# Optimization experiments

Hardware: AMD Instinct MI355X
Metric: run time of the kernel (lower is better)

Reference implementation:

```python
import jax, jax.numpy as jnp
import numpy as np

RADIUS = 6
KERNEL = 2 * RADIUS + 1  # 13
TEMPERATURE = 0.07
EPS = 1e-12  # F.normalize eps


def setup_inputs() -> dict:
    key = jax.random.key(0)
    k1, k2 = jax.random.split(key)
    B, C, H, W = 4, 256, 128, 128
    f_a = jax.random.normal(k1, (B, C, H, W), dtype=jnp.float32)
    f_b = jax.random.normal(k2, (B, C, H, W), dtype=jnp.float32)
    return {"f_a": f_a, "f_b": f_b}


def _l2_normalize(x):
    # matches F.normalize(x, dim=1): x / max(||x||_2, eps)
    n = jnp.sqrt(jnp.sum(x * x, axis=1, keepdims=True))
    return x / jnp.maximum(n, EPS)


def reference(f_a, f_b):
    a = _l2_normalize(f_a)
    b = _l2_normalize(f_b)
    b_pad = jnp.pad(b, ((0, 0), (0, 0), (RADIUS, RADIUS), (RADIUS, RADIUS)))

    # offsets in the same (row-major ky, kx) order as F.unfold
    ky, kx = jnp.meshgrid(jnp.arange(KERNEL), jnp.arange(KERNEL), indexing="ij")
    offsets = jnp.stack([ky.ravel(), kx.ravel()], axis=-1)  # [K^2, 2]

    shape = f_a.shape  # (B, C, H, W)

    def step(carry, off):
        shifted = jax.lax.dynamic_slice(b_pad, (0, 0, off[0], off[1]), shape)
        c = jnp.einsum("bchw,bchw->bhw", a, shifted)
        return carry, c

    _, corr = jax.lax.scan(step, None, offsets)  # [K^2, B, H, W]
    corr = jnp.transpose(corr, (1, 0, 2, 3)) / TEMPERATURE  # [B, K^2, H, W]
    return corr
```

## Files before the change

### kernel.cpp

```cpp
#include <hip/hip_runtime.h>
#include <stdint.h>


typedef _Float16 half8 __attribute__((ext_vector_type(8)));
typedef _Float16 half2v __attribute__((ext_vector_type(2)));
typedef float floatx4 __attribute__((ext_vector_type(4)));

#define B_ 4
#define C_ 256
#define H_ 128
#define W_ 128
#define K2_ 169
#define INV_T 14.285714285714286f
#define KGS (H_ * W_ * 32)

static __device__ __forceinline__ void gload16(const void* g, void* l) {
  __builtin_amdgcn_global_load_lds((const __attribute__((address_space(1))) void*)g,
                                   (__attribute__((address_space(3))) void*)l, 16, 0, 0);
}

__global__ __launch_bounds__(256, 4) void nt_kernel(const float* __restrict__ fa,
                                                    const float* __restrict__ fb,
                                                    _Float16* __restrict__ an,
                                                    _Float16* __restrict__ bn) {
  __shared__ _Float16 tile[256 * 66];
  __shared__ float ps[16 * 64];
  __shared__ float invn[64];
  const int bid = blockIdx.x;
  const int wh = bid & 1, h = (bid >> 1) & 127, bb = (bid >> 8) & 3, tens = bid >> 10;
  const float* __restrict__ src = tens ? fb : fa;
  _Float16* __restrict__ dst = tens ? bn : an;
  const int t = threadIdx.x;
  const int f = t & 15, cp = t >> 4;

  const float* gs = src + (((size_t)bb * C_ + cp) * H_ + h) * W_ + wh * 64 + f * 4;

  floatx4 v[16];
  #pragma unroll
  for (int it = 0; it < 16; ++it)
    v[it] = *(const floatx4*)(gs + (size_t)it * 16 * H_ * W_);

  floatx4 ss0 = {0.f, 0.f, 0.f, 0.f}, ss1 = {0.f, 0.f, 0.f, 0.f};
  #pragma unroll
  for (int it = 0; it < 16; ++it) {
    if (it & 1) ss1 += v[it] * v[it]; else ss0 += v[it] * v[it];
    const int c = it * 16 + cp;
    const int s8 = ((c >> 5) & 7) * 8;
    _Float16* wp = tile + c * 66 + ((f * 4) ^ s8);
    half2v p0 = {(_Float16)v[it].x, (_Float16)v[it].y};
    half2v p1 = {(_Float16)v[it].z, (_Float16)v[it].w};
    *(half2v*)wp = p0;
    *(half2v*)(wp + 2) = p1;
  }
  const floatx4 ss = ss0 + ss1;
  *(floatx4*)(ps + cp * 64 + f * 4) = ss;
  __syncthreads();
  if (t < 64) {
    float s2 = 0.f;
    #pragma unroll
    for (int p = 0; p < 16; ++p) s2 += ps[p * 64 + t];
    invn[t] = 1.0f / fmaxf(sqrtf(s2), 1e-12f);
  }
  __syncthreads();

  const int seg = t >> 5, pr = t & 31;
  const float sc = tens ? 1.0f : INV_T;
  const float inv0 = invn[2 * pr] * sc, inv1 = invn[2 * pr + 1] * sc;
  const int ppr = pr ^ (4 * seg);
  _Float16 o0[32] __attribute__((aligned(16)));
  _Float16 o1[32] __attribute__((aligned(16)));
  #pragma unroll
  for (int j = 0; j < 32; ++j) {
    const int c = seg * 32 + j;
    const half2v d = *(const half2v*)(tile + c * 66 + ppr * 2);
    o0[j] = (_Float16)((float)d.x * inv0);
    o1[j] = (_Float16)((float)d.y * inv1);
  }
  _Float16* dp = dst + ((((size_t)bb * 8 + seg) * H_ + h) * W_ + wh * 64 + 2 * pr) * 32;
  #pragma unroll
  for (int q4 = 0; q4 < 4; ++q4) {
    *(uint4*)(dp + q4 * 8) = *(const uint4*)(o0 + q4 * 8);
    *(uint4*)(dp + 32 + q4 * 8) = *(const uint4*)(o1 + q4 * 8);
  }
}

union SmemU { _Float16 stage[2][16384]; float ostage[K2_ * 2 * 17]; };

__global__ __launch_bounds__(512, 4) void corr_kernel(const _Float16* __restrict__ an,
                                                      const _Float16* __restrict__ bn,
                                                      float* __restrict__ out) {
  __shared__ SmemU u;
  const int bid = blockIdx.x;
  const int xcd = bid & 7, l = bid >> 3;
  const int bb = l >> 5, hseg = (l >> 3) & 3, wt = l & 7;
  const int hg = xcd * 4 + hseg;
  const int h0 = hg * 4, w0 = wt * 16;
  const int t = threadIdx.x;
  const int lane = t & 63, wv = t >> 6;
  const int ml = lane & 15, q = lane >> 4;
  const int ntile = wv & 1, jjg = wv >> 1;

  const _Float16* ptr[4];
  unsigned flags = 0u;
  #pragma unroll
  for (int j = 0; j < 4; ++j) {
    const int job = j * 512 + t;
    if (job < 1792) {
      const int row = job / 112, rem = job - row * 112;
      const int col = rem >> 2, qt = rem & 3;
      const int rim = h0 - 6 + row, cim = w0 - 6 + col;
      const bool ok = ((unsigned)rim < (unsigned)H_) && ((unsigned)cim < (unsigned)W_);
      ptr[j] = bn + (((size_t)bb * 8 * H_ + (ok ? rim : 0)) * W_ + (ok ? cim : 0)) * 32 + qt * 8;
      if (ok) flags |= 1u << j;
    } else {
      const int aj = job - 1792;
      const int px = aj >> 2, qt = aj & 3;
      const int r = px >> 4, m = px & 15;
      ptr[j] = an + (((size_t)bb * 8 * H_ + h0 + r) * W_ + w0 + m) * 32 + qt * 8;
      flags |= 1u << j;
    }
  }

  const uint4 z4 = make_uint4(0u, 0u, 0u, 0u);
  #pragma unroll
  for (int j = 0; j < 4; ++j) {
    *(uint4*)((char*)u.stage[0] + (j * 512 + t) * 16) = z4;
    *(uint4*)((char*)u.stage[1] + (j * 512 + t) * 16) = z4;
  }
  __syncthreads();

  #pragma unroll
  for (int j = 0; j < 4; ++j) {
    if (flags & (1u << j))
      gload16(ptr[j], (char*)u.stage[0] + (j * 512 + wv * 64) * 16);
    ptr[j] += KGS;
  }

  floatx4 acc[4][4] = {};

  for (int kg = 0; kg < 8; ++kg) {
    __syncthreads();
    if (kg < 7) {
      char* nb = (char*)u.stage[(kg + 1) & 1];
      #pragma unroll
      for (int j = 0; j < 4; ++j) {
        if (flags & (1u << j))
          gload16(ptr[j], nb + (j * 512 + wv * 64) * 16);
        ptr[j] += KGS;
      }
    }
    const _Float16* sb = u.stage[kg & 1];

    half8 A[4];
    #pragma unroll
    for (int r = 0; r < 4; ++r)
      A[r] = *(const half8*)(sb + 14336 + (r * 16 + ml) * 32 + q * 8);

    #pragma unroll
    for (int uu = 0; uu < 4; ++uu) {
      const int jj = jjg + 4 * uu;
      const half8 Bf = *(const half8*)(sb + jj * 896 + (ntile * 16 + ml) * 32 + q * 8);
      #pragma unroll
      for (int r = 0; r < 4; ++r) {
        if ((uu == 0 && r > jjg) || (uu == 3 && r < jjg)) continue;
        acc[uu][r] = __builtin_amdgcn_mfma_f32_16x16x32_f16(A[r], Bf, acc[uu][r], 0, 0, 0);
      }
    }
  }

  #pragma unroll
  for (int r2 = 0; r2 < 2; ++r2) {
    if (r2) __syncthreads();
    #pragma unroll
    for (int uu = 0; uu < 4; ++uu) {
      const int jj = jjg + 4 * uu;
      const int col = ntile * 16 + ml;
      #pragma unroll
      for (int rr = 2 * r2; rr < 2 * r2 + 2; ++rr) {
        if ((uu == 0 && rr > jjg) || (uu == 3 && rr < jjg)) continue;
        const int dy6 = jj - rr;
        #pragma unroll
        for (int p = 0; p < 4; ++p) {
          const int ip = q * 4 + p;
          const int dx6 = col - ip;
          if (dx6 >= 0 && dx6 <= 12)
            u.ostage[((dy6 * 13 + dx6) * 2 + (rr & 1)) * 17 + ip] = acc[uu][rr][p];
        }
      }
    }
    __syncthreads();
    for (int s = t; s < K2_ * 32; s += 512) {
      const int k = s >> 5, r1 = (s >> 4) & 1, ip = s & 15;
      out[(((size_t)bb * K2_ + k) * H_ + h0 + 2 * r2 + r1) * W_ + w0 + ip] =
          u.ostage[(k * 2 + r1) * 17 + ip];
    }
  }
}

extern "C" void kernel_launch(void* const* d_in, const int* in_sizes, int n_in,
                              void* d_out, int out_size, void* d_ws, size_t ws_size,
                              hipStream_t stream) {
  const float* fa = (const float*)d_in[0];
  const float* fb = (const float*)d_in[1];
  float* out = (float*)d_out;
  _Float16* an = (_Float16*)d_ws;
  _Float16* bn = an + (size_t)B_ * H_ * W_ * C_;
  nt_kernel<<<2048, 256, 0, stream>>>(fa, fb, an, bn);
  corr_kernel<<<1024, 512, 0, stream>>>(an, bn, out);
}
```

Before: 201.9 us.

## Split normalize-transpose into a norm-reduction pass and an LDS-free normalize pass

The single LDS-tiled normalize-and-transpose kernel is replaced by two kernels. The first computes partial per-pixel sums of squares over 32-channel slices and writes them to scratch placed in the unused tail of the output buffer, which the correlation kernel later overwrites. The second sums those partials, scales, converts to fp16 and writes the channel-blocked layout directly from registers, with no shared memory and more blocks. This is meant to raise occupancy and drop the LDS round trip and barriers. In exchange the fp32 inputs are read twice, there is extra partial-sum traffic, and an extra kernel launch.

New measurement: 219.6 us. +8.7%, slower.

```diff
diff --git a/kernel.cpp b/kernel.cpp
--- a/kernel.cpp
+++ b/kernel.cpp
@@ -3,7 +3,6 @@
 
 
 typedef _Float16 half8 __attribute__((ext_vector_type(8)));
-typedef _Float16 half2v __attribute__((ext_vector_type(2)));
 typedef float floatx4 __attribute__((ext_vector_type(4)));
 
 #define B_ 4
@@ -13,74 +12,65 @@
 #define K2_ 169
 #define INV_T 14.285714285714286f
 #define KGS (H_ * W_ * 32)
+#define HW_ (H_ * W_)
+#define P_OFF 40108032
 
 static __device__ __forceinline__ void gload16(const void* g, void* l) {
   __builtin_amdgcn_global_load_lds((const __attribute__((address_space(1))) void*)g,
                                    (__attribute__((address_space(3))) void*)l, 16, 0, 0);
 }
 
-__global__ __launch_bounds__(256, 4) void nt_kernel(const float* __restrict__ fa,
-                                                    const float* __restrict__ fb,
-                                                    _Float16* __restrict__ an,
-                                                    _Float16* __restrict__ bn) {
-  __shared__ _Float16 tile[256 * 66];
-  __shared__ float ps[16 * 64];
-  __shared__ float invn[64];
+__global__ __launch_bounds__(256, 8) void norm_kernel(const float* __restrict__ fa,
+                                                      const float* __restrict__ fb,
+                                                      float* __restrict__ P) {
   const int bid = blockIdx.x;
-  const int wh = bid & 1, h = (bid >> 1) & 127, bb = (bid >> 8) & 3, tens = bid >> 10;
+  const int rg = bid & 15, cs = (bid >> 4) & 7, bb = (bid >> 7) & 3, tens = bid >> 9;
+  const float* __restrict__ src = tens ? fb : fa;
+  const int t = threadIdx.x;
+  const float* gs = src + ((size_t)bb * C_ + cs * 32) * HW_ + rg * 1024 + t * 4;
+  floatx4 acc = {0.f, 0.f, 0.f, 0.f};
+  #pragma unroll
+  for (int cc = 0; cc < 32; ++cc) {
+    const floatx4 v = *(const floatx4*)(gs + (size_t)cc * HW_);
+    acc += v * v;
+  }
+  *(floatx4*)(P + ((((size_t)tens * 4 + bb) * 8 + cs) * HW_) + rg * 1024 + t * 4) = acc;
+}
+
+__global__ __launch_bounds__(256, 6) void nt2_kernel(const float* __restrict__ fa,
+                                                     const float* __restrict__ fb,
+                                                     const float* __restrict__ P,
+                                                     _Float16* __restrict__ an,
+                                                     _Float16* __restrict__ bn) {
+  const int bid = blockIdx.x;
+  const int rg = bid & 63, kg = (bid >> 6) & 7, bb = (bid >> 9) & 3, tens = bid >> 11;
   const float* __restrict__ src = tens ? fb : fa;
   _Float16* __restrict__ dst = tens ? bn : an;
   const int t = threadIdx.x;
-  const int f = t & 15, cp = t >> 4;
-
-  const float* gs = src + (((size_t)bb * C_ + cp) * H_ + h) * W_ + wh * 64 + f * 4;
-
-  floatx4 v[16];
-  #pragma unroll
-  for (int it = 0; it < 16; ++it)
-    v[it] = *(const floatx4*)(gs + (size_t)it * 16 * H_ * W_);
-
-  floatx4 ss0 = {0.f, 0.f, 0.f, 0.f}, ss1 = {0.f, 0.f, 0.f, 0.f};
-  #pragma unroll
-  for (int it = 0; it < 16; ++it) {
-    if (it & 1) ss1 += v[it] * v[it]; else ss0 += v[it] * v[it];
-    const int c = it * 16 + cp;
-    const int s8 = ((c >> 5) & 7) * 8;
-    _Float16* wp = tile + c * 66 + ((f * 4) ^ s8);
-    half2v p0 = {(_Float16)v[it].x, (_Float16)v[it].y};
-    half2v p1 = {(_Float16)v[it].z, (_Float16)v[it].w};
-    *(half2v*)wp = p0;
-    *(half2v*)(wp + 2) = p1;
-  }
-  const floatx4 ss = ss0 + ss1;
-  *(floatx4*)(ps + cp * 64 + f * 4) = ss;
-  __syncthreads();
-  if (t < 64) {
-    float s2 = 0.f;
-    #pragma unroll
-    for (int p = 0; p < 16; ++p) s2 += ps[p * 64 + t];
-    invn[t] = 1.0f / fmaxf(sqrtf(s2), 1e-12f);
-  }
-  __syncthreads();
-
-  const int seg = t >> 5, pr = t & 31;
+  const int w = t >> 6, l = t & 63, pxg = l >> 2, ccg = l & 3;
+  const int pxq = rg * 256 + w * 64 + pxg * 4;
+
+  const float* Pb = P + (((size_t)tens * 4 + bb) * 8) * HW_ + pxq;
+  floatx4 s = {0.f, 0.f, 0.f, 0.f};
+  #pragma unroll
+  for (int cs = 0; cs < 8; ++cs) s += *(const floatx4*)(Pb + (size_t)cs * HW_);
   const float sc = tens ? 1.0f : INV_T;
-  const float inv0 = invn[2 * pr] * sc, inv1 = invn[2 * pr + 1] * sc;
-  const int ppr = pr ^ (4 * seg);
-  _Float16 o0[32] __attribute__((aligned(16)));
-  _Float16 o1[32] __attribute__((aligned(16)));
-  #pragma unroll
-  for (int j = 0; j < 32; ++j) {
-    const int c = seg * 32 + j;
-    const half2v d = *(const half2v*)(tile + c * 66 + ppr * 2);
-    o0[j] = (_Float16)((float)d.x * inv0);
-    o1[j] = (_Float16)((float)d.y * inv1);
-  }
-  _Float16* dp = dst + ((((size_t)bb * 8 + seg) * H_ + h) * W_ + wh * 64 + 2 * pr) * 32;
-  #pragma unroll
-  for (int q4 = 0; q4 < 4; ++q4) {
-    *(uint4*)(dp + q4 * 8) = *(const uint4*)(o0 + q4 * 8);
-    *(uint4*)(dp + 32 + q4 * 8) = *(const uint4*)(o1 + q4 * 8);
+  float inv[4];
+  #pragma unroll
+  for (int j = 0; j < 4; ++j) inv[j] = sc / fmaxf(sqrtf(s[j]), 1e-12f);
+
+  const float* gs = src + ((size_t)bb * C_ + kg * 32 + ccg * 8) * HW_ + pxq;
+  floatx4 v[8];
+  #pragma unroll
+  for (int cc = 0; cc < 8; ++cc) v[cc] = *(const floatx4*)(gs + (size_t)cc * HW_);
+
+  _Float16* db = dst + ((size_t)bb * 8 + kg) * (size_t)HW_ * 32;
+  #pragma unroll
+  for (int j = 0; j < 4; ++j) {
+    half8 h;
+    #pragma unroll
+    for (int cc = 0; cc < 8; ++cc) h[cc] = (_Float16)(v[cc][j] * inv[j]);
+    *(half8*)(db + (size_t)(pxq + j) * 32 + ccg * 8) = h;
   }
 }
 
@@ -203,8 +193,10 @@
   const float* fa = (const float*)d_in[0];
   const float* fb = (const float*)d_in[1];
   float* out = (float*)d_out;
+  float* P = (float*)((char*)d_out + P_OFF);
   _Float16* an = (_Float16*)d_ws;
   _Float16* bn = an + (size_t)B_ * H_ * W_ * C_;
-  nt_kernel<<<2048, 256, 0, stream>>>(fa, fb, an, bn);
+  norm_kernel<<<1024, 256, 0, stream>>>(fa, fb, P);
+  nt2_kernel<<<4096, 256, 0, stream>>>(fa, fb, P, an, bn);
   corr_kernel<<<1024, 512, 0, stream>>>(an, bn, out);
 }
```
